# Kernel optimization log

Measured on AMD Instinct MI355X. Metric: run time of the kernel, lower is better.

## Reference

```python
import jax, jax.numpy as jnp
import numpy as np

B = 8388608  # batch

def moth(x, a, b):
    # per-feature parametric elementwise activation: a * x * sigmoid(b * x)
    return a * x * jax.nn.sigmoid(b * x)

def setup_inputs() -> dict:
    key = jax.random.key(0)
    ks = jax.random.split(key, 12)
    inp = {
        'x':  jax.random.normal(ks[0], (B, 2), dtype=jnp.float32),
        'W1': jax.random.normal(ks[1], (2, 8), dtype=jnp.float32) * (1.0 / np.sqrt(2)),
        'b1': jax.random.normal(ks[2], (8,), dtype=jnp.float32) * 0.01,
        'a1': jax.random.normal(ks[3], (8,), dtype=jnp.float32) * 0.1 + 1.0,
        'c1': jax.random.normal(ks[4], (8,), dtype=jnp.float32) * 0.1 + 1.0,
        'W2': jax.random.normal(ks[5], (8, 4), dtype=jnp.float32) * (1.0 / np.sqrt(8)),
        'b2': jax.random.normal(ks[6], (4,), dtype=jnp.float32) * 0.01,
        'a2': jax.random.normal(ks[7], (4,), dtype=jnp.float32) * 0.1 + 1.0,
        'c2': jax.random.normal(ks[8], (4,), dtype=jnp.float32) * 0.1 + 1.0,
        'W3': jax.random.normal(ks[9], (4, 1), dtype=jnp.float32) * (1.0 / np.sqrt(4)),
        'b3': jax.random.normal(ks[10], (1,), dtype=jnp.float32) * 0.01,
    }
    return inp

def reference(x, W1, b1, a1, c1, W2, b2, a2, c2, W3, b3):
    h = x @ W1 + b1            # [B, 8]
    h = moth(h, a1, c1)        # [B, 8]
    h = h @ W2 + b2            # [B, 4]
    h = moth(h, a2, c2)        # [B, 4]
    out = h @ W3 + b3          # [B, 1]
    return out
```

## Files before the change

kernel.cpp:

```cpp
#include <hip/hip_runtime.h>

#define NLOG2E -1.44269504088896340736f

typedef float f32x2 __attribute__((ext_vector_type(2)));


__global__ void prefold_kernel(
    const float* __restrict__ W1, const float* __restrict__ b1,
    const float* __restrict__ a1, const float* __restrict__ c1,
    const float* __restrict__ W2, const float* __restrict__ b2,
    const float* __restrict__ a2, const float* __restrict__ c2,
    const float* __restrict__ W3, const float* __restrict__ b3,
    float* __restrict__ C)
{
    if (threadIdx.x == 0 && blockIdx.x == 0) {
        for (int j = 0; j < 8; ++j) {
            float ncl = c1[j] * NLOG2E;
            C[j]      = W1[j]     * ncl;
            C[8 + j]  = W1[8 + j] * ncl;
            C[16 + j] = b1[j]     * ncl;
            float k1 = a1[j] / ncl;
            for (int k = 0; k < 4; ++k)
                C[24 + j * 4 + k] = W2[j * 4 + k] * k1;
        }
        for (int k = 0; k < 4; ++k) {
            C[56 + k] = b2[k];
            C[60 + k] = c2[k] * NLOG2E;
            C[64 + k] = a2[k] * W3[k];
        }
        C[68] = b3[0];
    }
}

__global__ __launch_bounds__(256, 4) void PlaygroundModel_66365834658304_kernel(
    const float* __restrict__ x, const float* __restrict__ C,
    float* __restrict__ out, int rows)
{
    const f32x2* Cp  = (const f32x2*)C;
    float bb3 = C[68];

    int tid = blockIdx.x * blockDim.x + threadIdx.x;
    long long base = (long long)tid * 4;

    if (base + 3 < rows) {
        const float4* x4 = (const float4*)x;
        float4 p0 = x4[(size_t)tid * 2 + 0];
        float4 p1 = x4[(size_t)tid * 2 + 1];
        float X0[4] = {p0.x, p0.z, p1.x, p1.z};
        float X1[4] = {p0.y, p0.w, p1.y, p1.w};

        f32x2 u[4][4];
#pragma unroll
        for (int r = 0; r < 4; ++r) {
            f32x2 x0b = {X0[r], X0[r]};
            f32x2 x1b = {X1[r], X1[r]};
#pragma unroll
            for (int p = 0; p < 4; ++p)
                u[r][p] = __builtin_elementwise_fma(
                              x0b, Cp[p],
                              __builtin_elementwise_fma(x1b, Cp[4 + p],
                                                        Cp[8 + p]));
        }

#pragma unroll
        for (int r = 0; r < 4; ++r)
#pragma unroll
            for (int p = 0; p < 4; ++p) {
                f32x2 e;
                e[0] = __builtin_amdgcn_exp2f(u[r][p][0]);
                e[1] = __builtin_amdgcn_exp2f(u[r][p][1]);
                f32x2 d = e + 1.0f;
                f32x2 s;
                s[0] = __builtin_amdgcn_rcpf(d[0]);
                s[1] = __builtin_amdgcn_rcpf(d[1]);
                u[r][p] *= s;
            }

        f32x2 t2a[4], t2b[4];
#pragma unroll
        for (int r = 0; r < 4; ++r) {
            f32x2 ta = Cp[28], tb = Cp[29];
#pragma unroll
            for (int j = 0; j < 8; ++j) {
                float hj = u[r][j >> 1][j & 1];
                f32x2 hb = {hj, hj};
                ta = __builtin_elementwise_fma(hb, Cp[12 + j * 2 + 0], ta);
                tb = __builtin_elementwise_fma(hb, Cp[12 + j * 2 + 1], tb);
            }
            t2a[r] = ta; t2b[r] = tb;
        }

        float res[4];
#pragma unroll
        for (int r = 0; r < 4; ++r) {
            f32x2 u2a = Cp[30] * t2a[r];
            f32x2 u2b = Cp[31] * t2b[r];
            f32x2 ea, eb;
            ea[0] = __builtin_amdgcn_exp2f(u2a[0]);
            ea[1] = __builtin_amdgcn_exp2f(u2a[1]);
            eb[0] = __builtin_amdgcn_exp2f(u2b[0]);
            eb[1] = __builtin_amdgcn_exp2f(u2b[1]);
            f32x2 da = ea + 1.0f, db = eb + 1.0f;
            f32x2 sa, sb;
            sa[0] = __builtin_amdgcn_rcpf(da[0]);
            sa[1] = __builtin_amdgcn_rcpf(da[1]);
            sb[0] = __builtin_amdgcn_rcpf(db[0]);
            sb[1] = __builtin_amdgcn_rcpf(db[1]);
            f32x2 pa = t2a[r] * sa;
            f32x2 pb = t2b[r] * sb;
            f32x2 acc = {bb3, 0.0f};
            acc = __builtin_elementwise_fma(pa, Cp[32], acc);
            acc = __builtin_elementwise_fma(pb, Cp[33], acc);
            res[r] = acc[0] + acc[1];
        }
        ((float4*)out)[tid] = make_float4(res[0], res[1], res[2], res[3]);
    } else if (base < rows) {
        const float* uw0  = C;
        const float* uw1  = C + 8;
        const float* ub   = C + 16;
        const float* w2f  = C + 24;
        const float* bb2  = C + 56;
        const float* ncl2 = C + 60;
        const float* aw2  = C + 64;
        for (long long rr = base; rr < rows; ++rr) {
            float x0 = x[rr * 2 + 0], x1 = x[rr * 2 + 1];
            float h[8];
#pragma unroll
            for (int j = 0; j < 8; ++j) {
                float uu = fmaf(x0, uw0[j], fmaf(x1, uw1[j], ub[j]));
                float s  = __builtin_amdgcn_rcpf(
                               1.0f + __builtin_amdgcn_exp2f(uu));
                h[j] = uu * s;
            }
            float o = bb3;
#pragma unroll
            for (int k = 0; k < 4; ++k) {
                float t = bb2[k];
#pragma unroll
                for (int j = 0; j < 8; ++j) t = fmaf(h[j], w2f[j * 4 + k], t);
                float u2 = ncl2[k] * t;
                float sg = __builtin_amdgcn_rcpf(
                               1.0f + __builtin_amdgcn_exp2f(u2));
                o = fmaf(t * sg, aw2[k], o);
            }
            out[rr] = o;
        }
    }
}

extern "C" void kernel_launch(void* const* d_in, const int* in_sizes, int n_in,
                              void* d_out, int out_size, void* d_ws, size_t ws_size,
                              hipStream_t stream) {
    const float* x  = (const float*)d_in[0];
    const float* W1 = (const float*)d_in[1];
    const float* b1 = (const float*)d_in[2];
    const float* a1 = (const float*)d_in[3];
    const float* c1 = (const float*)d_in[4];
    const float* W2 = (const float*)d_in[5];
    const float* b2 = (const float*)d_in[6];
    const float* a2 = (const float*)d_in[7];
    const float* c2 = (const float*)d_in[8];
    const float* W3 = (const float*)d_in[9];
    const float* b3 = (const float*)d_in[10];
    float* out = (float*)d_out;
    float* C   = (float*)d_ws;

    prefold_kernel<<<1, 64, 0, stream>>>(W1, b1, a1, c1, W2, b2, a2, c2,
                                         W3, b3, C);

    int rows  = in_sizes[0] / 2;
    int rows4 = (rows + 3) / 4;
    int block = 256;
    int grid  = (rows4 + block - 1) / block;

    PlaygroundModel_66365834658304_kernel<<<grid, block, 0, stream>>>(
        x, C, out, rows);
}
```

Before: 125.5 us.

## Convert to persistent grid-stride loop with software-prefetched loads and nontemporal stores

Replaces the one-thread-per-four-rows launch with a fixed grid of 2048 blocks. Each thread walks a grid-stride loop and loads the next iteration's input while computing the current one. It also fuses the layer-2 and layer-3 loops, raises the occupancy hint in launch bounds, and writes outputs with nontemporal stores. The aim is to hide memory latency and cut block launch overhead on a bandwidth-bound elementwise MLP. The cost is that the tail rows are handled serially by thread 0, and register pressure from the prefetch may limit occupancy.

```diff
diff --git a/kernel.cpp b/kernel.cpp
--- a/kernel.cpp
+++ b/kernel.cpp
@@ -3,6 +3,7 @@
 #define NLOG2E -1.44269504088896340736f
 
 typedef float f32x2 __attribute__((ext_vector_type(2)));
+typedef float f32x4 __attribute__((ext_vector_type(4)));
 
 
 __global__ void prefold_kernel(
@@ -32,34 +33,45 @@
     }
 }
 
-__global__ __launch_bounds__(256, 4) void PlaygroundModel_66365834658304_kernel(
+__global__ __launch_bounds__(256, 8) void PlaygroundModel_66365834658304_kernel(
     const float* __restrict__ x, const float* __restrict__ C,
-    float* __restrict__ out, int rows)
+    float* __restrict__ out, int units, int rows, int T)
 {
-    const f32x2* Cp  = (const f32x2*)C;
+    const f32x2* Cp = (const f32x2*)C;
     float bb3 = C[68];
 
     int tid = blockIdx.x * blockDim.x + threadIdx.x;
-    long long base = (long long)tid * 4;
+    const f32x4* x4 = (const f32x4*)x;
+    f32x4* o4 = (f32x4*)out;
 
-    if (base + 3 < rows) {
-        const float4* x4 = (const float4*)x;
-        float4 p0 = x4[(size_t)tid * 2 + 0];
-        float4 p1 = x4[(size_t)tid * 2 + 1];
-        float X0[4] = {p0.x, p0.z, p1.x, p1.z};
-        float X1[4] = {p0.y, p0.w, p1.y, p1.w};
+    int u = tid;
+    f32x4 n0, n1;
+    if (u < units) {
+        n0 = x4[(size_t)u * 2 + 0];
+        n1 = x4[(size_t)u * 2 + 1];
+    }
+    while (u < units) {
+        f32x4 c0 = n0, c1 = n1;
+        int nu = u + T;
+        if (nu < units) {
+            n0 = x4[(size_t)nu * 2 + 0];
+            n1 = x4[(size_t)nu * 2 + 1];
+        }
 
-        f32x2 u[4][4];
+        float X0[4] = {c0.x, c0.z, c1.x, c1.z};
+        float X1[4] = {c0.y, c0.w, c1.y, c1.w};
+
+        f32x2 uv[4][4];
 #pragma unroll
         for (int r = 0; r < 4; ++r) {
             f32x2 x0b = {X0[r], X0[r]};
             f32x2 x1b = {X1[r], X1[r]};
 #pragma unroll
             for (int p = 0; p < 4; ++p)
-                u[r][p] = __builtin_elementwise_fma(
-                              x0b, Cp[p],
-                              __builtin_elementwise_fma(x1b, Cp[4 + p],
-                                                        Cp[8 + p]));
+                uv[r][p] = __builtin_elementwise_fma(
+                               x0b, Cp[p],
+                               __builtin_elementwise_fma(x1b, Cp[4 + p],
+                                                         Cp[8 + p]));
         }
 
 #pragma unroll
@@ -67,34 +79,28 @@
 #pragma unroll
             for (int p = 0; p < 4; ++p) {
                 f32x2 e;
-                e[0] = __builtin_amdgcn_exp2f(u[r][p][0]);
-                e[1] = __builtin_amdgcn_exp2f(u[r][p][1]);
+                e[0] = __builtin_amdgcn_exp2f(uv[r][p][0]);
+                e[1] = __builtin_amdgcn_exp2f(uv[r][p][1]);
                 f32x2 d = e + 1.0f;
                 f32x2 s;
                 s[0] = __builtin_amdgcn_rcpf(d[0]);
                 s[1] = __builtin_amdgcn_rcpf(d[1]);
-                u[r][p] *= s;
+                uv[r][p] *= s;
             }
 
-        f32x2 t2a[4], t2b[4];
+        float res[4];
 #pragma unroll
         for (int r = 0; r < 4; ++r) {
             f32x2 ta = Cp[28], tb = Cp[29];
 #pragma unroll
             for (int j = 0; j < 8; ++j) {
-                float hj = u[r][j >> 1][j & 1];
+                float hj = uv[r][j >> 1][j & 1];
                 f32x2 hb = {hj, hj};
                 ta = __builtin_elementwise_fma(hb, Cp[12 + j * 2 + 0], ta);
                 tb = __builtin_elementwise_fma(hb, Cp[12 + j * 2 + 1], tb);
             }
-            t2a[r] = ta; t2b[r] = tb;
-        }
-
-        float res[4];
-#pragma unroll
-        for (int r = 0; r < 4; ++r) {
-            f32x2 u2a = Cp[30] * t2a[r];
-            f32x2 u2b = Cp[31] * t2b[r];
+            f32x2 u2a = Cp[30] * ta;
+            f32x2 u2b = Cp[31] * tb;
             f32x2 ea, eb;
             ea[0] = __builtin_amdgcn_exp2f(u2a[0]);
             ea[1] = __builtin_amdgcn_exp2f(u2a[1]);
@@ -106,15 +112,19 @@
             sa[1] = __builtin_amdgcn_rcpf(da[1]);
             sb[0] = __builtin_amdgcn_rcpf(db[0]);
             sb[1] = __builtin_amdgcn_rcpf(db[1]);
-            f32x2 pa = t2a[r] * sa;
-            f32x2 pb = t2b[r] * sb;
+            f32x2 pa = ta * sa;
+            f32x2 pb = tb * sb;
             f32x2 acc = {bb3, 0.0f};
             acc = __builtin_elementwise_fma(pa, Cp[32], acc);
             acc = __builtin_elementwise_fma(pb, Cp[33], acc);
             res[r] = acc[0] + acc[1];
         }
-        ((float4*)out)[tid] = make_float4(res[0], res[1], res[2], res[3]);
-    } else if (base < rows) {
+        f32x4 ov = {res[0], res[1], res[2], res[3]};
+        __builtin_nontemporal_store(ov, &o4[u]);
+        u = nu;
+    }
+
+    if (tid == 0) {
         const float* uw0  = C;
         const float* uw1  = C + 8;
         const float* ub   = C + 16;
@@ -122,7 +132,7 @@
         const float* bb2  = C + 56;
         const float* ncl2 = C + 60;
         const float* aw2  = C + 64;
-        for (long long rr = base; rr < rows; ++rr) {
+        for (long long rr = (long long)units * 4; rr < rows; ++rr) {
             float x0 = x[rr * 2 + 0], x1 = x[rr * 2 + 1];
             float h[8];
 #pragma unroll
@@ -169,10 +179,11 @@
                                          W3, b3, C);
 
     int rows  = in_sizes[0] / 2;
-    int rows4 = (rows + 3) / 4;
+    int units = rows / 4;
     int block = 256;
-    int grid  = (rows4 + block - 1) / block;
+    int grid  = 2048;
+    int T     = grid * block;
 
     PlaygroundModel_66365834658304_kernel<<<grid, block, 0, stream>>>(
-        x, C, out, rows);
+        x, C, out, units, rows, T);
 }
```

New measurement: 131.9 us. 1.05x slower.
